# Kernel optimization log

Measured on AMD Instinct MI355X. Metric: run time of the kernel, lower is better.

The kernel has to match this reference:

```python
import jax, jax.numpy as jnp
import numpy as np

D_MODEL = 1024
H = 16
D_K = D_MODEL // H

def setup_inputs() -> dict:
    key = jax.random.key(0)
    ks = jax.random.split(key, 12)
    B, L = 2, 2048
    s = 1.0 / np.sqrt(D_MODEL)
    return {
        "query": jax.random.normal(ks[0], (B, L, D_MODEL), jnp.float32),
        "key":   jax.random.normal(ks[1], (B, L, D_MODEL), jnp.float32),
        "value": jax.random.normal(ks[2], (B, L, D_MODEL), jnp.float32),
        "Wq": jax.random.normal(ks[3], (D_MODEL, D_MODEL), jnp.float32) * s,
        "bq": jnp.zeros((D_MODEL,), jnp.float32),
        "Wk": jax.random.normal(ks[4], (D_MODEL, D_MODEL), jnp.float32) * s,
        "bk": jnp.zeros((D_MODEL,), jnp.float32),
        "Wv": jax.random.normal(ks[5], (D_MODEL, D_MODEL), jnp.float32) * s,
        "bv": jnp.zeros((D_MODEL,), jnp.float32),
        "Wo": jax.random.normal(ks[6], (D_MODEL, D_MODEL), jnp.float32) * s,
        "bo": jnp.zeros((D_MODEL,), jnp.float32),
    }

def reference(query, key, value, Wq, bq, Wk, bk, Wv, bv, Wo, bo):
    B, Lq, _ = query.shape
    Lk = key.shape[1]
    # projections (torch Linear: x @ W.T + b)
    q = query @ Wq.T + bq
    k = key   @ Wk.T + bk
    v = value @ Wv.T + bv
    # split heads: [B, H, L, d_k]
    q = q.reshape(B, Lq, H, D_K).transpose(0, 2, 1, 3)
    k = k.reshape(B, Lk, H, D_K).transpose(0, 2, 1, 3)
    v = v.reshape(B, Lk, H, D_K).transpose(0, 2, 1, 3)
    scores = jnp.einsum('bhqd,bhkd->bhqk', q, k) / jnp.sqrt(jnp.float32(D_K)).astype(q.dtype)
    attention_weight = jax.nn.softmax(scores, axis=-1)
    out = jnp.einsum('bhqk,bhkd->bhqd', attention_weight, v)
    out = out.transpose(0, 2, 1, 3).reshape(B, Lq, D_MODEL)
    output = out @ Wo.T + bo
    return (output, attention_weight)
```

## Files before the change

### kernel.cpp

```cpp
#include <hip/hip_runtime.h>
#include <hip/hip_bf16.h>
#include <math.h>

#define NHEAD 16
#define DK 64
#define SEQL 2048
#define NBATCH 2
#define DMODEL 1024
#define MROWS 4096

typedef __attribute__((ext_vector_type(4))) float floatx4;
typedef __attribute__((ext_vector_type(8))) short short8;
typedef __attribute__((ext_vector_type(4))) short short4v;

__device__ __forceinline__ short f2bf(float f) {
    __hip_bfloat16 h = __float2bfloat16(f);
    return *reinterpret_cast<short*>(&h);
}

__device__ __forceinline__ void gll16(const void* g, void* l) {
    __builtin_amdgcn_global_load_lds(
        (const __attribute__((address_space(1))) void*)g,
        (__attribute__((address_space(3))) void*)l, 16, 0, 0);
}

__global__ void cvt_bf16(const float* __restrict__ in, short* __restrict__ out, int n4) {
    int i = blockIdx.x * 256 + threadIdx.x;
    if (i < n4) {
        float4 f = ((const float4*)in)[i];
        short4v v;
        v.x = f2bf(f.x); v.y = f2bf(f.y); v.z = f2bf(f.z); v.w = f2bf(f.w);
        ((short4v*)out)[i] = v;
    }
}

template<int MODE>
__global__ __launch_bounds__(256, 2)
void gemm_bt(const short* __restrict__ A, const short* __restrict__ W,
             const float* __restrict__ bias, void* __restrict__ Out) {
    __shared__ __align__(16) short As[128 * 32];
    __shared__ __align__(16) short Bs[128 * 32];
    const int t = threadIdx.x;
    const int lane = t & 63;
    const int w = t >> 6;
    const int wr = w >> 1, wc = w & 1;
    const int quad = lane >> 4;
    const int l16 = lane & 15;
    const int bm = blockIdx.y * 128;
    const int bn = blockIdx.x * 128;

    floatx4 acc[4][4];
#pragma unroll
    for (int i = 0; i < 4; ++i)
#pragma unroll
        for (int j = 0; j < 4; ++j) acc[i][j] = (floatx4){0.f, 0.f, 0.f, 0.f};

    for (int k0 = 0; k0 < 1024; k0 += 32) {
        __syncthreads();
#pragma unroll
        for (int i = 0; i < 2; ++i) {
            int c = i * 256 + t;
            int row = c >> 2, kk = (c & 3) * 8;
            gll16(A + (size_t)(bm + row) * 1024 + k0 + kk, (char*)As + c * 16);
            gll16(W + (size_t)(bn + row) * 1024 + k0 + kk, (char*)Bs + c * 16);
        }
        __syncthreads();
        short8 af[4], bfr[4];
#pragma unroll
        for (int ms = 0; ms < 4; ++ms)
            af[ms] = *(const short8*)&As[(wr * 64 + ms * 16 + l16) * 32 + quad * 8];
#pragma unroll
        for (int ns = 0; ns < 4; ++ns)
            bfr[ns] = *(const short8*)&Bs[(wc * 64 + ns * 16 + l16) * 32 + quad * 8];
#pragma unroll
        for (int ms = 0; ms < 4; ++ms)
#pragma unroll
            for (int ns = 0; ns < 4; ++ns)
                acc[ms][ns] = __builtin_amdgcn_mfma_f32_16x16x32_bf16(
                    af[ms], bfr[ns], acc[ms][ns], 0, 0, 0);
    }

#pragma unroll
    for (int ms = 0; ms < 4; ++ms) {
#pragma unroll
        for (int ns = 0; ns < 4; ++ns) {
            int n = bn + wc * 64 + ns * 16 + l16;
            float bv = bias[n];
#pragma unroll
            for (int r = 0; r < 4; ++r) {
                int m = bm + wr * 64 + ms * 16 + quad * 4 + r;
                float v = acc[ms][ns][r] + bv;
                if (MODE == 2) {
                    ((float*)Out)[(size_t)m * 1024 + n] = v;
                } else {
                    int b = m >> 11, l = m & 2047;
                    int h = n >> 6, d = n & 63;
                    short* o = (short*)Out;
                    if (MODE == 0)
                        o[(((size_t)(b * 16 + h) * 2048 + l) * 64) + d] = f2bf(v);
                    else
                        o[(((size_t)(b * 16 + h) * 64 + d) * 2048) + l] = f2bf(v);
                }
            }
        }
    }
}

__global__ __launch_bounds__(256, 2)
void attn_kernel(const short* __restrict__ Qh, const short* __restrict__ Kh,
                 const short* __restrict__ Vt, float* __restrict__ P,
                 short* __restrict__ Ows) {
    __shared__ __align__(16) short Qs[2 * 64 * 32];
    __shared__ __align__(16) short Ks[2 * 64 * 32];
    __shared__ __align__(16) short Vs[2 * 64 * 32];
    __shared__ __align__(16) short Ps[2 * 64 * 32];

    const int t = threadIdx.x;
    const int lane = t & 63;
    const int w = t >> 6;
    const int quad = lane >> 4;
    const int l16 = lane & 15;
    const int qt = blockIdx.x;
    const int bh = blockIdx.y;
    const size_t qkBase = (size_t)bh * SEQL * DK;

#pragma unroll
    for (int i = 0; i < 2; ++i) {
        int c = i * 256 + t;
        int ks = c >> 8, r = (c >> 2) & 63, c4 = c & 3;
        gll16(Qh + qkBase + (size_t)(qt * 64 + r) * 64 + ks * 32 + c4 * 8,
              (char*)Qs + c * 16);
    }
    __syncthreads();
    short8 aq[2];
    aq[0] = *(const short8*)&Qs[0 * 2048 + (w * 16 + l16) * 32 + quad * 8];
    aq[1] = *(const short8*)&Qs[1 * 2048 + (w * 16 + l16) * 32 + quad * 8];

    float mrow[4], lrow[4];
#pragma unroll
    for (int r = 0; r < 4; ++r) { mrow[r] = -INFINITY; lrow[r] = 0.f; }

    for (int kt = 0; kt < 32; ++kt) {
        __syncthreads();
#pragma unroll
        for (int i = 0; i < 2; ++i) {
            int c = i * 256 + t;
            int ks = c >> 8, r = (c >> 2) & 63, c4 = c & 3;
            gll16(Kh + qkBase + (size_t)(kt * 64 + r) * 64 + ks * 32 + c4 * 8,
                  (char*)Ks + c * 16);
        }
        __syncthreads();
        floatx4 s[4];
#pragma unroll
        for (int ns = 0; ns < 4; ++ns) s[ns] = (floatx4){0.f, 0.f, 0.f, 0.f};
#pragma unroll
        for (int ks = 0; ks < 2; ++ks)
#pragma unroll
            for (int ns = 0; ns < 4; ++ns) {
                short8 b = *(const short8*)&Ks[ks * 2048 + (ns * 16 + l16) * 32 + quad * 8];
                s[ns] = __builtin_amdgcn_mfma_f32_16x16x32_bf16(aq[ks], b, s[ns], 0, 0, 0);
            }
#pragma unroll
        for (int ns = 0; ns < 4; ++ns) s[ns] *= 0.125f;

        float tm[4], sum[4];
#pragma unroll
        for (int r = 0; r < 4; ++r)
            tm[r] = fmaxf(fmaxf(s[0][r], s[1][r]), fmaxf(s[2][r], s[3][r]));
#pragma unroll
        for (int off = 1; off < 16; off <<= 1)
#pragma unroll
            for (int r = 0; r < 4; ++r)
                tm[r] = fmaxf(tm[r], __shfl_xor(tm[r], off, 64));
#pragma unroll
        for (int r = 0; r < 4; ++r) {
            float mnew = fmaxf(mrow[r], tm[r]);
            tm[r] = mnew;
            sum[r] = __expf(s[0][r] - mnew) + __expf(s[1][r] - mnew) +
                     __expf(s[2][r] - mnew) + __expf(s[3][r] - mnew);
        }
#pragma unroll
        for (int off = 1; off < 16; off <<= 1)
#pragma unroll
            for (int r = 0; r < 4; ++r)
                sum[r] += __shfl_xor(sum[r], off, 64);
#pragma unroll
        for (int r = 0; r < 4; ++r) {
            lrow[r] = lrow[r] * __expf(mrow[r] - tm[r]) + sum[r];
            mrow[r] = tm[r];
        }
    }

    float inv_l[4];
#pragma unroll
    for (int r = 0; r < 4; ++r) inv_l[r] = 1.f / lrow[r];

    floatx4 oacc[4];
#pragma unroll
    for (int i = 0; i < 4; ++i) oacc[i] = (floatx4){0.f, 0.f, 0.f, 0.f};

    for (int kt = 0; kt < 32; ++kt) {
        __syncthreads();
#pragma unroll
        for (int i = 0; i < 2; ++i) {
            int c = i * 256 + t;
            int ks = c >> 8, r = (c >> 2) & 63, c4 = c & 3;
            gll16(Kh + qkBase + (size_t)(kt * 64 + r) * 64 + ks * 32 + c4 * 8,
                  (char*)Ks + c * 16);
            gll16(Vt + qkBase + (size_t)r * 2048 + kt * 64 + ks * 32 + c4 * 8,
                  (char*)Vs + c * 16);
        }
        __syncthreads();
        floatx4 s[4];
#pragma unroll
        for (int ns = 0; ns < 4; ++ns) s[ns] = (floatx4){0.f, 0.f, 0.f, 0.f};
#pragma unroll
        for (int ks = 0; ks < 2; ++ks)
#pragma unroll
            for (int ns = 0; ns < 4; ++ns) {
                short8 b = *(const short8*)&Ks[ks * 2048 + (ns * 16 + l16) * 32 + quad * 8];
                s[ns] = __builtin_amdgcn_mfma_f32_16x16x32_bf16(aq[ks], b, s[ns], 0, 0, 0);
            }
        const size_t prowbase = ((size_t)bh * SEQL + qt * 64 + w * 16) * SEQL + kt * 64;
#pragma unroll
        for (int ns = 0; ns < 4; ++ns) {
#pragma unroll
            for (int r = 0; r < 4; ++r) {
                float p = __expf(s[ns][r] * 0.125f - mrow[r]) * inv_l[r];
                int lr16 = quad * 4 + r;
                P[prowbase + (size_t)lr16 * SEQL + ns * 16 + l16] = p;
                int col = ns * 16 + l16;
                Ps[(col >> 5) * 2048 + (w * 16 + lr16) * 32 + (col & 31)] = f2bf(p);
            }
        }
        __syncthreads();
#pragma unroll
        for (int ks = 0; ks < 2; ++ks) {
            short8 pa = *(const short8*)&Ps[ks * 2048 + (w * 16 + l16) * 32 + quad * 8];
#pragma unroll
            for (int ds = 0; ds < 4; ++ds) {
                short8 b = *(const short8*)&Vs[ks * 2048 + (ds * 16 + l16) * 32 + quad * 8];
                oacc[ds] = __builtin_amdgcn_mfma_f32_16x16x32_bf16(pa, b, oacc[ds], 0, 0, 0);
            }
        }
    }

    const int b = bh >> 4, h = bh & 15;
#pragma unroll
    for (int ds = 0; ds < 4; ++ds) {
        int d = h * 64 + ds * 16 + l16;
#pragma unroll
        for (int r = 0; r < 4; ++r) {
            int q = qt * 64 + w * 16 + quad * 4 + r;
            Ows[(size_t)(b * 2048 + q) * 1024 + d] = f2bf(oacc[ds][r]);
        }
    }
}

extern "C" void kernel_launch(void* const* d_in, const int* in_sizes, int n_in,
                              void* d_out, int out_size, void* d_ws, size_t ws_size,
                              hipStream_t stream) {
    const float* query = (const float*)d_in[0];
    const float* key   = (const float*)d_in[1];
    const float* value = (const float*)d_in[2];
    const float* Wq = (const float*)d_in[3];
    const float* bq = (const float*)d_in[4];
    const float* Wk = (const float*)d_in[5];
    const float* bk = (const float*)d_in[6];
    const float* Wv = (const float*)d_in[7];
    const float* bv = (const float*)d_in[8];
    const float* Wo = (const float*)d_in[9];
    const float* bo = (const float*)d_in[10];

    float* out0  = (float*)d_out;
    float* attnW = out0 + (size_t)MROWS * DMODEL;

    short* ws  = (short*)d_ws;
    short* xq  = ws;
    short* xk  = xq + 4194304;
    short* xv  = xk + 4194304;
    short* wqb = xv + 4194304;
    short* wkb = wqb + 1048576;
    short* wvb = wkb + 1048576;
    short* wob = wvb + 1048576;
    short* qh  = wob + 1048576;
    short* kh  = qh + 4194304;
    short* vt  = kh + 4194304;
    short* ows = vt + 4194304;

    cvt_bf16<<<4096, 256, 0, stream>>>(query, xq, 1048576);
    cvt_bf16<<<4096, 256, 0, stream>>>(key,   xk, 1048576);
    cvt_bf16<<<4096, 256, 0, stream>>>(value, xv, 1048576);
    cvt_bf16<<<1024, 256, 0, stream>>>(Wq, wqb, 262144);
    cvt_bf16<<<1024, 256, 0, stream>>>(Wk, wkb, 262144);
    cvt_bf16<<<1024, 256, 0, stream>>>(Wv, wvb, 262144);
    cvt_bf16<<<1024, 256, 0, stream>>>(Wo, wob, 262144);

    dim3 gg(8, 32);
    gemm_bt<0><<<gg, 256, 0, stream>>>(xq, wqb, bq, qh);
    gemm_bt<0><<<gg, 256, 0, stream>>>(xk, wkb, bk, kh);
    gemm_bt<1><<<gg, 256, 0, stream>>>(xv, wvb, bv, vt);

    attn_kernel<<<dim3(32, 32), 256, 0, stream>>>(qh, kh, vt, attnW, ows);

    gemm_bt<2><<<gg, 256, 0, stream>>>(ows, wob, bo, out0);
}
```

Before: 837.9 us.

## Load attention operands directly from global memory and drop max-subtraction softmax

Removes the shared-memory staging of Q, K and V, so each wave loads its MFMA operands straight from global memory and most block-wide barriers go away. The first pass now accumulates exp2 sums with no running max, assuming scores are small enough not to overflow, and the second pass reuses that unnormalised exponent. Probability stores become nontemporal, the only barrier left is a wave-local LDS waitcnt for the per-wave P tile, and launch bounds rise to three blocks per CU. The risks are overflow on inputs with large scores, more redundant global and L2 traffic because each wave reloads the K and V tiles, and reliance on the P tile being written and read by the same wave.

```diff
diff --git a/kernel.cpp b/kernel.cpp
--- a/kernel.cpp
+++ b/kernel.cpp
@@ -106,13 +106,11 @@
     }
 }
 
-__global__ __launch_bounds__(256, 2)
+#define EXPSCALE 0.18033688f
+__global__ __launch_bounds__(256, 3)
 void attn_kernel(const short* __restrict__ Qh, const short* __restrict__ Kh,
                  const short* __restrict__ Vt, float* __restrict__ P,
                  short* __restrict__ Ows) {
-    __shared__ __align__(16) short Qs[2 * 64 * 32];
-    __shared__ __align__(16) short Ks[2 * 64 * 32];
-    __shared__ __align__(16) short Vs[2 * 64 * 32];
     __shared__ __align__(16) short Ps[2 * 64 * 32];
 
     const int t = threadIdx.x;
@@ -124,124 +122,93 @@
     const int bh = blockIdx.y;
     const size_t qkBase = (size_t)bh * SEQL * DK;
 
-#pragma unroll
-    for (int i = 0; i < 2; ++i) {
-        int c = i * 256 + t;
-        int ks = c >> 8, r = (c >> 2) & 63, c4 = c & 3;
-        gll16(Qh + qkBase + (size_t)(qt * 64 + r) * 64 + ks * 32 + c4 * 8,
-              (char*)Qs + c * 16);
-    }
-    __syncthreads();
     short8 aq[2];
-    aq[0] = *(const short8*)&Qs[0 * 2048 + (w * 16 + l16) * 32 + quad * 8];
-    aq[1] = *(const short8*)&Qs[1 * 2048 + (w * 16 + l16) * 32 + quad * 8];
-
-    float mrow[4], lrow[4];
-#pragma unroll
-    for (int r = 0; r < 4; ++r) { mrow[r] = -INFINITY; lrow[r] = 0.f; }
-
+    {
+        const short* qrow = Qh + qkBase + (size_t)(qt * 64 + w * 16 + l16) * 64;
+        aq[0] = *(const short8*)(qrow + quad * 8);
+        aq[1] = *(const short8*)(qrow + 32 + quad * 8);
+    }
+
+    float psum[4] = {0.f, 0.f, 0.f, 0.f};
+#pragma unroll 2
     for (int kt = 0; kt < 32; ++kt) {
-        __syncthreads();
-#pragma unroll
-        for (int i = 0; i < 2; ++i) {
-            int c = i * 256 + t;
-            int ks = c >> 8, r = (c >> 2) & 63, c4 = c & 3;
-            gll16(Kh + qkBase + (size_t)(kt * 64 + r) * 64 + ks * 32 + c4 * 8,
-                  (char*)Ks + c * 16);
-        }
-        __syncthreads();
+        const short* kb_base = Kh + qkBase + (size_t)kt * 64 * 64;
+        short8 kb[2][4];
+#pragma unroll
+        for (int ks = 0; ks < 2; ++ks)
+#pragma unroll
+            for (int ns = 0; ns < 4; ++ns)
+                kb[ks][ns] = *(const short8*)(kb_base + (size_t)(ns * 16 + l16) * 64 + ks * 32 + quad * 8);
         floatx4 s[4];
 #pragma unroll
         for (int ns = 0; ns < 4; ++ns) s[ns] = (floatx4){0.f, 0.f, 0.f, 0.f};
 #pragma unroll
         for (int ks = 0; ks < 2; ++ks)
 #pragma unroll
-            for (int ns = 0; ns < 4; ++ns) {
-                short8 b = *(const short8*)&Ks[ks * 2048 + (ns * 16 + l16) * 32 + quad * 8];
-                s[ns] = __builtin_amdgcn_mfma_f32_16x16x32_bf16(aq[ks], b, s[ns], 0, 0, 0);
-            }
-#pragma unroll
-        for (int ns = 0; ns < 4; ++ns) s[ns] *= 0.125f;
-
-        float tm[4], sum[4];
+            for (int ns = 0; ns < 4; ++ns)
+                s[ns] = __builtin_amdgcn_mfma_f32_16x16x32_bf16(aq[ks], kb[ks][ns], s[ns], 0, 0, 0);
+#pragma unroll
+        for (int ns = 0; ns < 4; ++ns)
+#pragma unroll
+            for (int r = 0; r < 4; ++r)
+                psum[r] += exp2f(s[ns][r] * EXPSCALE);
+    }
+#pragma unroll
+    for (int off = 1; off < 16; off <<= 1)
 #pragma unroll
         for (int r = 0; r < 4; ++r)
-            tm[r] = fmaxf(fmaxf(s[0][r], s[1][r]), fmaxf(s[2][r], s[3][r]));
-#pragma unroll
-        for (int off = 1; off < 16; off <<= 1)
-#pragma unroll
-            for (int r = 0; r < 4; ++r)
-                tm[r] = fmaxf(tm[r], __shfl_xor(tm[r], off, 64));
-#pragma unroll
-        for (int r = 0; r < 4; ++r) {
-            float mnew = fmaxf(mrow[r], tm[r]);
-            tm[r] = mnew;
-            sum[r] = __expf(s[0][r] - mnew) + __expf(s[1][r] - mnew) +
-                     __expf(s[2][r] - mnew) + __expf(s[3][r] - mnew);
-        }
-#pragma unroll
-        for (int off = 1; off < 16; off <<= 1)
-#pragma unroll
-            for (int r = 0; r < 4; ++r)
-                sum[r] += __shfl_xor(sum[r], off, 64);
-#pragma unroll
-        for (int r = 0; r < 4; ++r) {
-            lrow[r] = lrow[r] * __expf(mrow[r] - tm[r]) + sum[r];
-            mrow[r] = tm[r];
-        }
-    }
-
+            psum[r] += __shfl_xor(psum[r], off, 64);
     float inv_l[4];
 #pragma unroll
-    for (int r = 0; r < 4; ++r) inv_l[r] = 1.f / lrow[r];
+    for (int r = 0; r < 4; ++r) inv_l[r] = 1.f / psum[r];
 
     floatx4 oacc[4];
 #pragma unroll
     for (int i = 0; i < 4; ++i) oacc[i] = (floatx4){0.f, 0.f, 0.f, 0.f};
 
     for (int kt = 0; kt < 32; ++kt) {
-        __syncthreads();
-#pragma unroll
-        for (int i = 0; i < 2; ++i) {
-            int c = i * 256 + t;
-            int ks = c >> 8, r = (c >> 2) & 63, c4 = c & 3;
-            gll16(Kh + qkBase + (size_t)(kt * 64 + r) * 64 + ks * 32 + c4 * 8,
-                  (char*)Ks + c * 16);
-            gll16(Vt + qkBase + (size_t)r * 2048 + kt * 64 + ks * 32 + c4 * 8,
-                  (char*)Vs + c * 16);
-        }
-        __syncthreads();
+        const short* kb_base = Kh + qkBase + (size_t)kt * 64 * 64;
+        short8 kb[2][4];
+#pragma unroll
+        for (int ks = 0; ks < 2; ++ks)
+#pragma unroll
+            for (int ns = 0; ns < 4; ++ns)
+                kb[ks][ns] = *(const short8*)(kb_base + (size_t)(ns * 16 + l16) * 64 + ks * 32 + quad * 8);
+        short8 vb[2][4];
+#pragma unroll
+        for (int ks = 0; ks < 2; ++ks)
+#pragma unroll
+            for (int ds = 0; ds < 4; ++ds)
+                vb[ks][ds] = *(const short8*)(Vt + qkBase + (size_t)(ds * 16 + l16) * 2048 + kt * 64 + ks * 32 + quad * 8);
         floatx4 s[4];
 #pragma unroll
         for (int ns = 0; ns < 4; ++ns) s[ns] = (floatx4){0.f, 0.f, 0.f, 0.f};
 #pragma unroll
         for (int ks = 0; ks < 2; ++ks)
 #pragma unroll
-            for (int ns = 0; ns < 4; ++ns) {
-                short8 b = *(const short8*)&Ks[ks * 2048 + (ns * 16 + l16) * 32 + quad * 8];
-                s[ns] = __builtin_amdgcn_mfma_f32_16x16x32_bf16(aq[ks], b, s[ns], 0, 0, 0);
-            }
+            for (int ns = 0; ns < 4; ++ns)
+                s[ns] = __builtin_amdgcn_mfma_f32_16x16x32_bf16(aq[ks], kb[ks][ns], s[ns], 0, 0, 0);
+
         const size_t prowbase = ((size_t)bh * SEQL + qt * 64 + w * 16) * SEQL + kt * 64;
 #pragma unroll
         for (int ns = 0; ns < 4; ++ns) {
 #pragma unroll
             for (int r = 0; r < 4; ++r) {
-                float p = __expf(s[ns][r] * 0.125f - mrow[r]) * inv_l[r];
+                float p = exp2f(s[ns][r] * EXPSCALE) * inv_l[r];
                 int lr16 = quad * 4 + r;
-                P[prowbase + (size_t)lr16 * SEQL + ns * 16 + l16] = p;
+                __builtin_nontemporal_store(p, &P[prowbase + (size_t)lr16 * SEQL + ns * 16 + l16]);
                 int col = ns * 16 + l16;
                 Ps[(col >> 5) * 2048 + (w * 16 + lr16) * 32 + (col & 31)] = f2bf(p);
             }
         }
-        __syncthreads();
+        asm volatile("s_waitcnt lgkmcnt(0)" ::: "memory");
+        __builtin_amdgcn_sched_barrier(0);
 #pragma unroll
         for (int ks = 0; ks < 2; ++ks) {
             short8 pa = *(const short8*)&Ps[ks * 2048 + (w * 16 + l16) * 32 + quad * 8];
 #pragma unroll
-            for (int ds = 0; ds < 4; ++ds) {
-                short8 b = *(const short8*)&Vs[ks * 2048 + (ds * 16 + l16) * 32 + quad * 8];
-                oacc[ds] = __builtin_amdgcn_mfma_f32_16x16x32_bf16(pa, b, oacc[ds], 0, 0, 0);
-            }
+            for (int ds = 0; ds < 4; ++ds)
+                oacc[ds] = __builtin_amdgcn_mfma_f32_16x16x32_bf16(pa, vb[ks][ds], oacc[ds], 0, 0, 0);
         }
     }
 
```

Result: slower. 959.2 us (+14.5%).
